# Kernel tuning notes

Measured on AMD Instinct MI355X. Metric: run time of the kernel, lower is better.

Reference implementation:

```python
import jax, jax.numpy as jnp
import numpy as np

B, L, D, S = 4, 4096, 1024, 16
EPS = 1e-5  # nn.LayerNorm default


def setup_inputs() -> dict:
    key = jax.random.key(0)
    ks = jax.random.split(key, 8)
    s = 0.02
    return {
        "x_seq": jax.random.normal(ks[0], (B, L, D), jnp.float32),
        "h_prev": jnp.zeros((B, S), jnp.float32),
        "gamma": jnp.ones((D,), jnp.float32),
        "beta": jnp.zeros((D,), jnp.float32),
        "W_in": jax.random.normal(ks[1], (D, D), jnp.float32) * s,
        "b_in": jnp.zeros((D,), jnp.float32),
        "W_A": jax.random.normal(ks[2], (D, S), jnp.float32) * s,
        "b_A": jnp.zeros((S,), jnp.float32),
        "W_B": jax.random.normal(ks[3], (D, S), jnp.float32) * s,
        "b_B": jnp.zeros((S,), jnp.float32),
        "W_C": jax.random.normal(ks[4], (D, S), jnp.float32) * s,
        "b_C": jnp.zeros((S,), jnp.float32),
        "W_dt": jax.random.normal(ks[5], (D, 1), jnp.float32) * s,
        "b_dt": jnp.zeros((1,), jnp.float32),
        "W_out": jax.random.normal(ks[6], (D, D), jnp.float32) * s,
        "b_out": jnp.zeros((D,), jnp.float32),
    }


def _layernorm(x, gamma, beta):
    mu = jnp.mean(x, axis=-1, keepdims=True)
    var = jnp.mean(jnp.square(x - mu), axis=-1, keepdims=True)
    return (x - mu) * jax.lax.rsqrt(var + EPS) * gamma + beta


def reference(x_seq, h_prev, gamma, beta, W_in, b_in, W_A, b_A, W_B, b_B,
              W_C, b_C, W_dt, b_dt, W_out, b_out):
    # pre-scan projections (all batched over (B, L))
    x = _layernorm(x_seq, gamma, beta)
    x = jax.nn.silu(x @ W_in + b_in)                    # (B, L, D)
    log_A = -jax.nn.softplus(x @ W_A + b_A)             # (B, L, S)
    B_t = x @ W_B + b_B                                 # (B, L, S)
    C_t = x @ W_C + b_C                                 # (B, L, S)
    dt = jax.nn.softplus(x @ W_dt + b_dt)               # (B, L, 1)
    A_disc = jnp.exp(log_A * dt)                        # (B, L, S)
    u = jnp.mean(x, axis=-1, keepdims=True)             # (B, L, 1)
    Bu = (B_t * dt) * u                                 # (B, L, S)

    # selective scan: h_t = A_t * h_{t-1} + Bu_t  over time axis
    def step(h, inp):
        a_t, bu_t = inp
        h = a_t * h + bu_t
        return h, h

    h_final, hs = jax.lax.scan(
        step, h_prev,
        (jnp.swapaxes(A_disc, 0, 1), jnp.swapaxes(Bu, 0, 1)))
    hs = jnp.swapaxes(hs, 0, 1)                         # (B, L, S)

    y = jnp.sum(C_t * hs, axis=-1, keepdims=True)       # (B, L, 1)
    y_seq = (x * y) @ W_out + b_out + x_seq             # (B, L, D)
    return y_seq, h_final
```

## Files before the change

kernel.cpp:

```cpp
#include <hip/hip_runtime.h>

typedef unsigned short u16;
typedef unsigned int u32;
typedef __attribute__((ext_vector_type(8))) short short8;
typedef __attribute__((ext_vector_type(4))) float f32x4;

#define B_ 4
#define L_ 4096
#define D_ 1024
#define S_ 16
#define M_ (B_ * L_)
#define NBG 64
#define LC 64

__device__ __forceinline__ float b2f(u16 h) {
    unsigned u = ((unsigned)h) << 16;
    return __builtin_bit_cast(float, u);
}
__device__ __forceinline__ u16 f2b(float f) {
    unsigned u = __builtin_bit_cast(unsigned, f);
    u += 0x7fffu + ((u >> 16) & 1u);
    return (u16)(u >> 16);
}
__device__ __forceinline__ float softplus_f(float z) {
    return z > 20.f ? z : log1pf(__expf(z));
}
__device__ __forceinline__ void gload16(const u16* g, const u16* l) {
    __builtin_amdgcn_global_load_lds(
        (const __attribute__((address_space(1))) u32*)g,
        (__attribute__((address_space(3))) u32*)l, 16, 0, 0);
}

__global__ __launch_bounds__(256) void prep_kernel(
    const float* __restrict__ W0, u16* __restrict__ Wt0,
    const float* __restrict__ W1, u16* __restrict__ Wt1,
    const float* __restrict__ WA, const float* __restrict__ WB,
    const float* __restrict__ WC, const float* __restrict__ Wdt,
    u16* __restrict__ Wp) {
    int b = blockIdx.x, tid = threadIdx.x;
    if (b < 2048) {
        const float* W = (b >> 10) ? W1 : W0;
        u16* Wt = (b >> 10) ? Wt1 : Wt0;
        int by = (b >> 5) & 31, bx = b & 31;
        int x = tid & 31, ty = tid >> 5;
        __shared__ float t[32][33];
        for (int j = ty; j < 32; j += 8)
            t[j][x] = W[(size_t)(by * 32 + j) * D_ + bx * 32 + x];
        __syncthreads();
        for (int j = ty; j < 32; j += 8)
            Wt[(size_t)(bx * 32 + j) * D_ + by * 32 + x] = f2b(t[x][j]);
    } else {
        int idx = (b - 2048) * 256 + tid;
        int s = idx >> 10, k = idx & 1023;
        float v;
        if (s < 16)       v = WA[k * 16 + s];
        else if (s < 32)  v = WB[k * 16 + (s - 16)];
        else if (s < 48)  v = WC[k * 16 + (s - 32)];
        else if (s == 48) v = Wdt[k];
        else if (s == 49) v = 1.0f / 1024.0f;
        else              v = 0.f;
        Wp[idx] = f2b(v);
    }
}

__global__ __launch_bounds__(256) void ln_kernel(
    const float* __restrict__ x, const float* __restrict__ gamma,
    const float* __restrict__ beta, u16* __restrict__ out) {
    int row = blockIdx.x, tid = threadIdx.x;
    const float4 v = *(const float4*)&x[(size_t)row * D_ + tid * 4];
    float s = v.x + v.y + v.z + v.w;
    float q = v.x * v.x + v.y * v.y + v.z * v.z + v.w * v.w;
    for (int o = 32; o > 0; o >>= 1) { s += __shfl_down(s, o); q += __shfl_down(q, o); }
    __shared__ float ss[4], qq[4];
    int w = tid >> 6, lane = tid & 63;
    if (lane == 0) { ss[w] = s; qq[w] = q; }
    __syncthreads();
    if (tid == 0) {
        float S = ss[0] + ss[1] + ss[2] + ss[3];
        float Q = qq[0] + qq[1] + qq[2] + qq[3];
        float mu = S * (1.f / D_);
        float var = Q * (1.f / D_) - mu * mu;
        ss[0] = mu; qq[0] = rsqrtf(var + 1e-5f);
    }
    __syncthreads();
    float mu = ss[0], rs = qq[0];
    const float4 gv = *(const float4*)&gamma[tid * 4];
    const float4 bv = *(const float4*)&beta[tid * 4];
    ushort4 o4;
    o4.x = f2b((v.x - mu) * rs * gv.x + bv.x);
    o4.y = f2b((v.y - mu) * rs * gv.y + bv.y);
    o4.z = f2b((v.z - mu) * rs * gv.z + bv.z);
    o4.w = f2b((v.w - mu) * rs * gv.w + bv.w);
    *(ushort4*)&out[(size_t)row * D_ + tid * 4] = o4;
}

template <int EPI>
__global__ __launch_bounds__(256, 2) void gemm128(
    const u16* __restrict__ A, const u16* __restrict__ Bt,
    const float* __restrict__ bias, const float* __restrict__ resid,
    const float* __restrict__ yrow,
    u16* __restrict__ outB, float* __restrict__ outF,
    int M, int N, int K, int nTileN) {
    __shared__ u16 sm[32768];
    const int TILES = K >> 6;

    int nwg = gridDim.x;
    int bid = blockIdx.x;
    int swz = (bid & 7) * (nwg >> 3) + (bid >> 3);
    int bx = swz % nTileN, by = swz / nTileN;
    int rowBase = by * 128, colBase = bx * 128;

    int tid = threadIdx.x;
    int lane = tid & 63, w = tid >> 6;
    int wr = w >> 1, wc = w & 1;
    int lr = lane & 15, lg = lane >> 4;
    const unsigned woff = (unsigned)((lr * 32 + lg * 8) ^ ((lr & 8) ? 16 : 0));

    int r = lane >> 2;
    int chunk = (lane & 3) ^ ((r & 8) ? 2 : 0);
    const u16* gA = A  + (size_t)(rowBase + w * 32 + r) * K + chunk * 8;
    const u16* gB = Bt + (size_t)(colBase + w * 32 + r) * K + chunk * 8;
    const unsigned sA = (unsigned)(w * 4) * 512u;

#define STAGE(sbb, tau)                                                          \
    do {                                                                         \
        _Pragma("unroll")                                                        \
        for (int i = 0; i < 2; i++)                                              \
            _Pragma("unroll")                                                    \
            for (int kb = 0; kb < 2; kb++) {                                     \
                size_t _go = (size_t)i * 16 * K + (size_t)(tau) * 64 + kb * 32;  \
                unsigned _lo = (sbb) + sA + (unsigned)(i * 2 + kb) * 512u;       \
                gload16(gA + _go, &sm[_lo]);                                     \
                gload16(gB + _go, &sm[_lo + 8192u]);                             \
            }                                                                    \
    } while (0)

    f32x4 acc[4][4] = {};

    STAGE(0u, 0);
    asm volatile("s_waitcnt vmcnt(0)" ::: "memory");
    __builtin_amdgcn_s_barrier();

    for (int t = 0; t < TILES; ++t) {
        const unsigned bb = (unsigned)(t & 1) * 16384u;
        const unsigned nb = (unsigned)((t + 1) & 1) * 16384u;
        if (t + 1 < TILES) STAGE(nb, t + 1);
        short8 af[4][2], bf[4][2];
#pragma unroll
        for (int m = 0; m < 4; m++)
#pragma unroll
            for (int ks = 0; ks < 2; ks++)
                af[m][ks] = *(const short8*)&sm[bb + (unsigned)(((wr * 4 + m) << 1) + ks) * 512u + woff];
#pragma unroll
        for (int n = 0; n < 4; n++)
#pragma unroll
            for (int ks = 0; ks < 2; ks++)
                bf[n][ks] = *(const short8*)&sm[bb + 8192u + (unsigned)(((wc * 4 + n) << 1) + ks) * 512u + woff];
        __builtin_amdgcn_s_setprio(1);
#pragma unroll
        for (int ks = 0; ks < 2; ks++)
#pragma unroll
            for (int m = 0; m < 4; m++)
#pragma unroll
                for (int n = 0; n < 4; n++)
                    acc[m][n] = __builtin_amdgcn_mfma_f32_16x16x32_bf16(
                        af[m][ks], bf[n][ks], acc[m][n], 0, 0, 0);
        __builtin_amdgcn_s_setprio(0);
        if (t + 1 < TILES) asm volatile("s_waitcnt vmcnt(0)" ::: "memory");
        __builtin_amdgcn_s_barrier();
    }
#undef STAGE

    if (EPI == 1) {
        float bcol[4];
#pragma unroll
        for (int n = 0; n < 4; n++) bcol[n] = bias[colBase + wc * 64 + n * 16 + lr];
#pragma unroll
        for (int m = 0; m < 4; m++)
#pragma unroll
            for (int n = 0; n < 4; n++)
#pragma unroll
                for (int j = 0; j < 4; j++) {
                    int row = wr * 64 + m * 16 + lg * 4 + j;
                    int col = wc * 64 + n * 16 + lr;
                    float v = acc[m][n][j] + bcol[n];
                    v = v / (1.f + __expf(-v));
                    int cbs = (col >> 4) ^ lg;
                    sm[row * 128 + cbs * 16 + (col & 15)] = f2b(v);
                }
        __syncthreads();
        int rr = tid >> 1, half = tid & 1;
        u16* gout = outB + (size_t)(rowBase + rr) * N + colBase;
#pragma unroll
        for (int q = 0; q < 4; q++) {
            int cb = half * 4 + q;
            int cbs = cb ^ ((rr >> 2) & 3);
            *(uint4*)&gout[cb * 16] = *(const uint4*)&sm[rr * 128 + cbs * 16];
        }
    } else {
        float bcol[4];
#pragma unroll
        for (int n = 0; n < 4; n++) bcol[n] = bias[colBase + wc * 64 + n * 16 + lr];
#pragma unroll
        for (int m = 0; m < 4; m++) {
            float yr[4];
#pragma unroll
            for (int j = 0; j < 4; j++)
                yr[j] = yrow[rowBase + wr * 64 + m * 16 + lg * 4 + j];
#pragma unroll
            for (int n = 0; n < 4; n++)
#pragma unroll
                for (int j = 0; j < 4; j++) {
                    int row = rowBase + wr * 64 + m * 16 + lg * 4 + j;
                    int col = colBase + wc * 64 + n * 16 + lr;
                    size_t o = (size_t)row * N + col;
                    outF[o] = acc[m][n][j] * yr[j] + bcol[n] + resid[o];
                }
        }
    }
}

__global__ __launch_bounds__(256) void proj_kernel(
    const u16* __restrict__ X, const u16* __restrict__ Wp,
    const float* __restrict__ bA, const float* __restrict__ bB,
    const float* __restrict__ bC, const float* __restrict__ bdt,
    float* __restrict__ Ad, float* __restrict__ Bu, float* __restrict__ Ct) {
    __shared__ u16 Xs[2][64][32];
    __shared__ u16 Ws[2][64][32];
    int rowBase = blockIdx.x * 64;
    int tid = threadIdx.x, lane = tid & 63, w = tid >> 6;
    int lr = lane & 15, lg = lane >> 4;
    f32x4 acc[4] = {};
    const int sr = lane >> 2, sc = (lane & 3) * 8;
    const u16* gX = &X[(size_t)(rowBase + w * 16 + sr) * 1024 + sc];
    const u16* gW = &Wp[(size_t)(w * 16 + sr) * 1024 + sc];

#define PSTAGE(d, k0)                              \
    do {                                           \
        gload16(gX + (k0), &Xs[d][w * 16][0]);     \
        gload16(gW + (k0), &Ws[d][w * 16][0]);     \
    } while (0)

    PSTAGE(0, 0);
    __syncthreads();
    int cur = 0;
    for (int k0 = 0; k0 < 1024; k0 += 32) {
        if (k0 + 32 < 1024) PSTAGE(cur ^ 1, k0 + 32);
        short8 a = *(const short8*)&Xs[cur][w * 16 + lr][lg * 8];
#pragma unroll
        for (int n = 0; n < 4; n++) {
            short8 b = *(const short8*)&Ws[cur][n * 16 + lr][lg * 8];
            acc[n] = __builtin_amdgcn_mfma_f32_16x16x32_bf16(a, b, acc[n], 0, 0, 0);
        }
        __syncthreads();
        cur ^= 1;
    }
#undef PSTAGE
    float bdt0 = bdt[0];
#pragma unroll
    for (int j = 0; j < 4; j++) {
        int row = rowBase + w * 16 + lg * 4 + j;
        float dtr = __shfl(acc[3][j], lg * 16 + 0, 64);
        float uv  = __shfl(acc[3][j], lg * 16 + 1, 64);
        float dt = softplus_f(dtr + bdt0);
        float zA = acc[0][j] + bA[lr];
        float zB = acc[1][j] + bB[lr];
        float zC = acc[2][j] + bC[lr];
        size_t o = (size_t)row * 16 + lr;
        Ad[o] = __expf(-dt * softplus_f(zA));
        Bu[o] = zB * dt * uv;
        Ct[o] = zC;
    }
}

__global__ __launch_bounds__(1024) void scan_part1(
    const float* __restrict__ Ad, const float* __restrict__ Bu,
    float* __restrict__ Pb, float* __restrict__ Qb) {
    int b = blockIdx.x >> 6, g = blockIdx.x & 63;
    int tid = threadIdx.x;
    int s = tid & 15, c = tid >> 4;
    size_t idx = ((size_t)b * L_ + g * LC + c) * S_ + s;
    float a = Ad[idx], bu = Bu[idx];
    __shared__ float Ps[16][64], Qs[16][64];
    Ps[s][c] = a; Qs[s][c] = bu;
    __syncthreads();
    if (tid < 16) {
        float P = 1.f, Q = 0.f;
        for (int cc = 0; cc < 64; cc++) {
            float pa = Ps[tid][cc], qa = Qs[tid][cc];
            P = pa * P;
            Q = pa * Q + qa;
        }
        int o = (b * NBG + g) * S_ + tid;
        Pb[o] = P; Qb[o] = Q;
    }
}

__global__ __launch_bounds__(1024) void scan_part3(
    const float* __restrict__ Ad, const float* __restrict__ Bu,
    const float* __restrict__ Ct, const float* __restrict__ Pb,
    const float* __restrict__ Qb, const float* __restrict__ hprev,
    float* __restrict__ y, float* __restrict__ hfinal) {
    int b = blockIdx.x >> 6, g = blockIdx.x & 63;
    int tid = threadIdx.x;
    int s = tid & 15, c = tid >> 4;
    size_t idx = ((size_t)b * L_ + g * LC + c) * S_ + s;
    float a = Ad[idx], bu = Bu[idx];
    __shared__ float Ps[16][64], Qs[16][64], Hin[16][65];
    Ps[s][c] = a; Qs[s][c] = bu;
    __syncthreads();
    if (tid < 16) {
        float h = hprev[b * S_ + tid];
        for (int gg = 0; gg < g; gg++) {
            int o = (b * NBG + gg) * S_ + tid;
            h = Pb[o] * h + Qb[o];
        }
        for (int cc = 0; cc < 64; cc++) {
            Hin[tid][cc] = h;
            h = Ps[tid][cc] * h + Qs[tid][cc];
        }
        if (g == NBG - 1) hfinal[b * S_ + tid] = h;
    }
    __syncthreads();
    float h = a * Hin[s][c] + bu;
    float p = Ct[idx] * h;
    p += __shfl_xor(p, 1);
    p += __shfl_xor(p, 2);
    p += __shfl_xor(p, 4);
    p += __shfl_xor(p, 8);
    if (s == 0) y[(size_t)b * L_ + g * LC + c] = p;
}

extern "C" void kernel_launch(void* const* d_in, const int* in_sizes, int n_in,
                              void* d_out, int out_size, void* d_ws, size_t ws_size,
                              hipStream_t stream) {
    const float* x_seq  = (const float*)d_in[0];
    const float* h_prev = (const float*)d_in[1];
    const float* gamma  = (const float*)d_in[2];
    const float* beta   = (const float*)d_in[3];
    const float* W_in   = (const float*)d_in[4];
    const float* b_in   = (const float*)d_in[5];
    const float* W_A    = (const float*)d_in[6];
    const float* b_A    = (const float*)d_in[7];
    const float* W_B    = (const float*)d_in[8];
    const float* b_B    = (const float*)d_in[9];
    const float* W_C    = (const float*)d_in[10];
    const float* b_C    = (const float*)d_in[11];
    const float* W_dt   = (const float*)d_in[12];
    const float* b_dt   = (const float*)d_in[13];
    const float* W_out  = (const float*)d_in[14];
    const float* b_out  = (const float*)d_in[15];

    char* ws = (char*)d_ws;
    u16*   x_ln   = (u16*)(ws + 0);
    u16*   x      = (u16*)(ws + 33554432);
    u16*   Wt_in  = (u16*)(ws + 67108864);
    u16*   Wt_out = (u16*)(ws + 69206016);
    u16*   Wp     = (u16*)(ws + 71303168);
    float* Ad     = (float*)(ws + 71434240);
    float* Bu     = (float*)(ws + 72482816);
    float* Ct     = (float*)(ws + 73531392);
    float* yv     = (float*)(ws + 74579968);
    float* Pb     = (float*)(ws + 74645504);
    float* Qb     = (float*)(ws + 74661888);
    float* out    = (float*)d_out;

    prep_kernel<<<2304, 256, 0, stream>>>(W_in, Wt_in, W_out, Wt_out,
                                          W_A, W_B, W_C, W_dt, Wp);
    ln_kernel<<<M_, 256, 0, stream>>>(x_seq, gamma, beta, x_ln);
    gemm128<1><<<(M_ / 128) * (D_ / 128), 256, 0, stream>>>(
        x_ln, Wt_in, b_in, nullptr, nullptr, x, nullptr, M_, D_, D_, D_ / 128);
    proj_kernel<<<M_ / 64, 256, 0, stream>>>(x, Wp, b_A, b_B, b_C, b_dt, Ad, Bu, Ct);
    scan_part1<<<B_ * NBG, 1024, 0, stream>>>(Ad, Bu, Pb, Qb);
    scan_part3<<<B_ * NBG, 1024, 0, stream>>>(Ad, Bu, Ct, Pb, Qb, h_prev,
                                              yv, out + (size_t)M_ * D_);
    gemm128<2><<<(M_ / 128) * (D_ / 128), 256, 0, stream>>>(
        x, Wt_out, b_out, x_seq, yv, nullptr, out, M_, D_, D_, D_ / 128);
}
```

Before: 159.8 us.

## Load GEMM B operand directly from global and fuse scan chunk reduction into proj

The GEMM now stages only the A tile through LDS and has each wave read its B fragments straight from global memory. This halves the shared-memory footprint so three workgroups can fit per CU. Separately, the per-chunk scan prefix (P,Q) computation is folded into proj_kernel, which removes the scan_part1 launch and its re-read of Ad/Bu. The direct global B loads are not shared across waves and are issued at the top of each iteration without prefetch, so they may expose memory latency in exchange for the higher occupancy.

After: 218.1 us. 36.4% more time.

```diff
diff --git a/kernel.cpp b/kernel.cpp
--- a/kernel.cpp
+++ b/kernel.cpp
@@ -95,13 +95,13 @@
 }
 
 template <int EPI>
-__global__ __launch_bounds__(256, 2) void gemm128(
+__global__ __launch_bounds__(256, 3) void gemm128(
     const u16* __restrict__ A, const u16* __restrict__ Bt,
     const float* __restrict__ bias, const float* __restrict__ resid,
     const float* __restrict__ yrow,
     u16* __restrict__ outB, float* __restrict__ outF,
     int M, int N, int K, int nTileN) {
-    __shared__ u16 sm[32768];
+    __shared__ u16 sm[16384];
     const int TILES = K >> 6;
 
     int nwg = gridDim.x;
@@ -118,44 +118,44 @@
 
     int r = lane >> 2;
     int chunk = (lane & 3) ^ ((r & 8) ? 2 : 0);
-    const u16* gA = A  + (size_t)(rowBase + w * 32 + r) * K + chunk * 8;
-    const u16* gB = Bt + (size_t)(colBase + w * 32 + r) * K + chunk * 8;
+    const u16* gA = A + (size_t)(rowBase + w * 32 + r) * K + chunk * 8;
     const unsigned sA = (unsigned)(w * 4) * 512u;
 
-#define STAGE(sbb, tau)                                                          \
+    const u16* gBf = Bt + (size_t)(colBase + wc * 64 + lr) * K + lg * 8;
+    const size_t rowK16 = (size_t)16 * K;
+
+#define STAGE_A(sbb, tau)                                                        \
     do {                                                                         \
         _Pragma("unroll")                                                        \
         for (int i = 0; i < 2; i++)                                              \
             _Pragma("unroll")                                                    \
-            for (int kb = 0; kb < 2; kb++) {                                     \
-                size_t _go = (size_t)i * 16 * K + (size_t)(tau) * 64 + kb * 32;  \
-                unsigned _lo = (sbb) + sA + (unsigned)(i * 2 + kb) * 512u;       \
-                gload16(gA + _go, &sm[_lo]);                                     \
-                gload16(gB + _go, &sm[_lo + 8192u]);                             \
-            }                                                                    \
+            for (int kb = 0; kb < 2; kb++)                                       \
+                gload16(gA + (size_t)i * rowK16 + (size_t)(tau) * 64 + kb * 32,  \
+                        &sm[(sbb) + sA + (unsigned)(i * 2 + kb) * 512u]);        \
     } while (0)
 
     f32x4 acc[4][4] = {};
 
-    STAGE(0u, 0);
+    STAGE_A(0u, 0);
     asm volatile("s_waitcnt vmcnt(0)" ::: "memory");
     __builtin_amdgcn_s_barrier();
 
     for (int t = 0; t < TILES; ++t) {
-        const unsigned bb = (unsigned)(t & 1) * 16384u;
-        const unsigned nb = (unsigned)((t + 1) & 1) * 16384u;
-        if (t + 1 < TILES) STAGE(nb, t + 1);
-        short8 af[4][2], bf[4][2];
+        const unsigned bb = (unsigned)(t & 1) * 8192u;
+        const unsigned nb = (unsigned)((t + 1) & 1) * 8192u;
+        short8 bf[4][2];
+#pragma unroll
+        for (int n = 0; n < 4; n++)
+#pragma unroll
+            for (int ks = 0; ks < 2; ks++)
+                bf[n][ks] = *(const short8*)&gBf[(size_t)(n * 16) * K + t * 64 + ks * 32];
+        if (t + 1 < TILES) STAGE_A(nb, t + 1);
+        short8 af[4][2];
 #pragma unroll
         for (int m = 0; m < 4; m++)
 #pragma unroll
             for (int ks = 0; ks < 2; ks++)
                 af[m][ks] = *(const short8*)&sm[bb + (unsigned)(((wr * 4 + m) << 1) + ks) * 512u + woff];
-#pragma unroll
-        for (int n = 0; n < 4; n++)
-#pragma unroll
-            for (int ks = 0; ks < 2; ks++)
-                bf[n][ks] = *(const short8*)&sm[bb + 8192u + (unsigned)(((wc * 4 + n) << 1) + ks) * 512u + woff];
         __builtin_amdgcn_s_setprio(1);
 #pragma unroll
         for (int ks = 0; ks < 2; ks++)
@@ -169,7 +169,7 @@
         if (t + 1 < TILES) asm volatile("s_waitcnt vmcnt(0)" ::: "memory");
         __builtin_amdgcn_s_barrier();
     }
-#undef STAGE
+#undef STAGE_A
 
     if (EPI == 1) {
         float bcol[4];
@@ -224,9 +224,11 @@
     const u16* __restrict__ X, const u16* __restrict__ Wp,
     const float* __restrict__ bA, const float* __restrict__ bB,
     const float* __restrict__ bC, const float* __restrict__ bdt,
-    float* __restrict__ Ad, float* __restrict__ Bu, float* __restrict__ Ct) {
+    float* __restrict__ Ad, float* __restrict__ Bu, float* __restrict__ Ct,
+    float* __restrict__ Pb, float* __restrict__ Qb) {
     __shared__ u16 Xs[2][64][32];
     __shared__ u16 Ws[2][64][32];
+    __shared__ float Psh[64][17], Qsh[64][17];
     int rowBase = blockIdx.x * 64;
     int tid = threadIdx.x, lane = tid & 63, w = tid >> 6;
     int lr = lane & 15, lg = lane >> 4;
@@ -259,7 +261,8 @@
     float bdt0 = bdt[0];
 #pragma unroll
     for (int j = 0; j < 4; j++) {
-        int row = rowBase + w * 16 + lg * 4 + j;
+        int rl = w * 16 + lg * 4 + j;
+        int row = rowBase + rl;
         float dtr = __shfl(acc[3][j], lg * 16 + 0, 64);
         float uv  = __shfl(acc[3][j], lg * 16 + 1, 64);
         float dt = softplus_f(dtr + bdt0);
@@ -267,31 +270,23 @@
         float zB = acc[1][j] + bB[lr];
         float zC = acc[2][j] + bC[lr];
         size_t o = (size_t)row * 16 + lr;
-        Ad[o] = __expf(-dt * softplus_f(zA));
-        Bu[o] = zB * dt * uv;
+        float adv = __expf(-dt * softplus_f(zA));
+        float buv = zB * dt * uv;
+        Ad[o] = adv;
+        Bu[o] = buv;
         Ct[o] = zC;
-    }
-}
-
-__global__ __launch_bounds__(1024) void scan_part1(
-    const float* __restrict__ Ad, const float* __restrict__ Bu,
-    float* __restrict__ Pb, float* __restrict__ Qb) {
-    int b = blockIdx.x >> 6, g = blockIdx.x & 63;
-    int tid = threadIdx.x;
-    int s = tid & 15, c = tid >> 4;
-    size_t idx = ((size_t)b * L_ + g * LC + c) * S_ + s;
-    float a = Ad[idx], bu = Bu[idx];
-    __shared__ float Ps[16][64], Qs[16][64];
-    Ps[s][c] = a; Qs[s][c] = bu;
+        Psh[rl][lr] = adv;
+        Qsh[rl][lr] = buv;
+    }
     __syncthreads();
     if (tid < 16) {
         float P = 1.f, Q = 0.f;
-        for (int cc = 0; cc < 64; cc++) {
-            float pa = Ps[tid][cc], qa = Qs[tid][cc];
+        for (int rr = 0; rr < 64; rr++) {
+            float pa = Psh[rr][tid];
             P = pa * P;
-            Q = pa * Q + qa;
-        }
-        int o = (b * NBG + g) * S_ + tid;
+            Q = pa * Q + Qsh[rr][tid];
+        }
+        int o = blockIdx.x * S_ + tid;
         Pb[o] = P; Qb[o] = Q;
     }
 }
@@ -370,8 +365,8 @@
     ln_kernel<<<M_, 256, 0, stream>>>(x_seq, gamma, beta, x_ln);
     gemm128<1><<<(M_ / 128) * (D_ / 128), 256, 0, stream>>>(
         x_ln, Wt_in, b_in, nullptr, nullptr, x, nullptr, M_, D_, D_, D_ / 128);
-    proj_kernel<<<M_ / 64, 256, 0, stream>>>(x, Wp, b_A, b_B, b_C, b_dt, Ad, Bu, Ct);
-    scan_part1<<<B_ * NBG, 1024, 0, stream>>>(Ad, Bu, Pb, Qb);
+    proj_kernel<<<M_ / 64, 256, 0, stream>>>(x, Wp, b_A, b_B, b_C, b_dt,
+                                             Ad, Bu, Ct, Pb, Qb);
     scan_part3<<<B_ * NBG, 1024, 0, stream>>>(Ad, Bu, Ct, Pb, Qb, h_prev,
                                               yv, out + (size_t)M_ * D_);
     gemm128<2><<<(M_ / 128) * (D_ / 128), 256, 0, stream>>>(
```
